# Optimization experiments

Hardware: AMD Instinct MI355X
Metric: run time of the kernel (lower is better)

## Reference

```python
import jax, jax.numpy as jnp
import numpy as np

D = 1024    # n_embd
H = 16      # n_heads
HD = D // H # head_dim
E = 8       # n_experts
K = 2       # k_best
DFF = 4096  # expert hidden
EPS = 1e-6
TEMP = 1.0  # target_temperature


def rmsnorm(x, w):
    return x * jax.lax.rsqrt(jnp.mean(x * x, axis=-1, keepdims=True) + EPS) * w


def setup_inputs() -> dict:
    key = jax.random.key(0)
    ks = jax.random.split(key, 10)
    B, S = 2, 2048
    s = 0.02
    return {
        "x": jax.random.normal(ks[0], (B, S, D), jnp.float32),
        "attention_mask": jnp.ones((B, S), jnp.int32),
        "attn_norm_w": jnp.ones((D,), jnp.float32),
        "wq": jax.random.normal(ks[1], (D, D), jnp.float32) * s,
        "wk": jax.random.normal(ks[2], (D, D), jnp.float32) * s,
        "wv": jax.random.normal(ks[3], (D, D), jnp.float32) * s,
        "wo": jax.random.normal(ks[4], (D, D), jnp.float32) * s,
        "mlp_norm_w": jnp.ones((D,), jnp.float32),
        "router_w": jax.random.normal(ks[5], (D, E), jnp.float32) * s,
        "w1": jax.random.normal(ks[6], (E, D, DFF), jnp.float32) * s,
        "b1": jnp.zeros((E, DFF), jnp.float32),
        "w2": jax.random.normal(ks[7], (E, DFF, D), jnp.float32) * s,
        "b2": jnp.zeros((E, D), jnp.float32),
    }


def reference(x, attention_mask, attn_norm_w, wq, wk, wv, wo, mlp_norm_w,
              router_w, w1, b1, w2, b2):
    B, S, _ = x.shape
    # ---- attention sub-block ----
    residual = x
    h = rmsnorm(x, attn_norm_w)
    q = (h @ wq).reshape(B, S, H, HD).transpose(0, 2, 1, 3)  # bhsd
    k = (h @ wk).reshape(B, S, H, HD).transpose(0, 2, 1, 3)
    v = (h @ wv).reshape(B, S, H, HD).transpose(0, 2, 1, 3)
    scores = jnp.einsum('bhqd,bhkd->bhqk', q, k) / np.sqrt(HD).astype(np.float32)
    causal = jnp.tril(jnp.ones((S, S), bool))
    mask = causal[None, None, :, :] & (attention_mask[:, None, None, :] > 0)
    scores = jnp.where(mask, scores, jnp.float32(-1e9))
    attn = jax.nn.softmax(scores, axis=-1)
    o = jnp.einsum('bhqk,bhkd->bhqd', attn, v).transpose(0, 2, 1, 3).reshape(B, S, D) @ wo
    x = residual + o

    # ---- MoE sub-block ----
    residual = x
    h = rmsnorm(x, mlp_norm_w)
    logits = h @ router_w                        # (B,S,E)
    probs = jax.nn.softmax(logits / TEMP, axis=-1)
    top_k_scores, top_k_indices = jax.lax.top_k(probs, K)  # (B,S,K)
    sel = jax.nn.one_hot(top_k_indices, E, dtype=probs.dtype)  # (B,S,K,E)
    expert_counts = sel.sum(axis=(0, 1, 2))      # (E,)
    frac = expert_counts / (B * S * K)
    balancing_loss = E * jnp.sum(frac * probs.mean(axis=(0, 1)))

    T = B * S
    flat = h.reshape(T, D)
    # dense per-expert MLP over all tokens, then gather the routed slots
    hid = jax.nn.gelu(jnp.einsum('td,edf->etf', flat, w1) + b1[:, None, :])  # (E,T,DFF)
    all_y = jnp.einsum('etf,efd->etd', hid, w2) + b2[:, None, :]             # (E,T,D)
    idx = top_k_indices.reshape(T, K)
    expert_out = all_y[idx, jnp.arange(T)[:, None], :]  # (T,K,D)
    # faithful to torch: outputs.view(k, B, S, D) is a raw reinterpretation
    out = expert_out.reshape(K, B, S, D)
    w = top_k_scores.transpose(2, 0, 1)[..., None]  # (K,B,S,1)
    x = residual + (out * w).sum(axis=0)
    return (x, balancing_loss, expert_counts)
```

## Files before the change

kernel.cpp:

```cpp
#include <hip/hip_runtime.h>


typedef _Float16 f16;
typedef _Float16 f16x8 __attribute__((ext_vector_type(8)));
typedef _Float16 f16x4v __attribute__((ext_vector_type(4)));
typedef float f32x4 __attribute__((ext_vector_type(4)));

#define DMODEL 1024
#define NHEAD  16
#define HDIM   64
#define NEXP   8
#define DFFN   4096
#define NBATCH 2
#define NSEQ   2048
#define NTOK   4096
#define NPAIR  8192

#define OFF_WQKVT  0ull
#define OFF_WOT    6291456ull
#define OFF_W1T    8388608ull
#define OFF_W2T    75497472ull
#define OFF_HATTN  142606336ull
#define OFF_Q      150994944ull
#define OFF_K      159383552ull
#define OFF_VT     167772160ull
#define OFF_OC     176160768ull
#define OFF_XMID   184549376ull
#define OFF_HMLP   201326592ull
#define OFF_HID    209715200ull
#define OFF_Y      276824064ull
#define OFF_Y2     OFF_HATTN
#define OFF_LIST   310378496ull
#define OFF_METAE  310509568ull
#define OFF_METAP  310542336ull
#define OFF_METAS  310575104ull
#define OFF_BPSUM  310607872ull
#define OFF_CNT    310640640ull
#define OFF_PSUM   310640704ull
#define OFF_BASE   310640768ull

__device__ __forceinline__ void ldsAsync16(const void* g, void* l) {
  __builtin_amdgcn_global_load_lds((const __attribute__((address_space(1))) void*)g,
                                   (__attribute__((address_space(3))) void*)l, 16, 0, 0);
}

__global__ void transpose_cast_kernel(const float* __restrict__ src, f16* __restrict__ dst,
                                      int R, int C) {
  __shared__ float tile[32][33];
  const size_t zoff = (size_t)blockIdx.z * R * C;
  src += zoff; dst += zoff;
  int c0 = blockIdx.x * 32, r0 = blockIdx.y * 32;
  int tx = threadIdx.x, ty = threadIdx.y;
#pragma unroll
  for (int i = 0; i < 4; i++)
    tile[ty + i * 8][tx] = src[(size_t)(r0 + ty + i * 8) * C + c0 + tx];
  __syncthreads();
#pragma unroll
  for (int i = 0; i < 4; i++)
    dst[(size_t)(c0 + ty + i * 8) * R + r0 + tx] = (f16)tile[tx][ty + i * 8];
}

__global__ void rmsnorm_kernel(const float* __restrict__ x, const float* __restrict__ w,
                               f16* __restrict__ out) {
  int t = blockIdx.x, tid = threadIdx.x;
  float4 v = ((const float4*)(x + (size_t)t * DMODEL))[tid];
  float ss = v.x * v.x + v.y * v.y + v.z * v.z + v.w * v.w;
#pragma unroll
  for (int o = 32; o > 0; o >>= 1) ss += __shfl_down(ss, o);
  __shared__ float red[4];
  if ((tid & 63) == 0) red[tid >> 6] = ss;
  __syncthreads();
  float tot = red[0] + red[1] + red[2] + red[3];
  float rstd = rsqrtf(tot / (float)DMODEL + 1e-6f);
  float4 wv = ((const float4*)w)[tid];
  f16x4v o4;
  o4[0] = (f16)(v.x * rstd * wv.x);
  o4[1] = (f16)(v.y * rstd * wv.y);
  o4[2] = (f16)(v.z * rstd * wv.z);
  o4[3] = (f16)(v.w * rstd * wv.w);
  *(f16x4v*)(out + (size_t)t * DMODEL + tid * 4) = o4;
}

template <class EPI>
__device__ __forceinline__ void gemm128(const f16* aP0, const f16* aP1, const f16* aP2, const f16* aP3,
                                        const f16* bP0, const f16* bP1, const f16* bP2, const f16* bP3,
                                        int K, EPI epi) {
  __shared__ __align__(16) f16 sA[128 * 64];
  __shared__ __align__(16) f16 sB[128 * 64];
  const int tid = threadIdx.x;
  const int lane = tid & 63, wave = tid >> 6;
  const int wm = (wave >> 1) * 64, wn = (wave & 1) * 64;
  const int q4 = lane >> 4, l15 = lane & 15;
  const int sw = lane & 7;
  const f16* aP[4] = {aP0, aP1, aP2, aP3};
  const f16* bP[4] = {bP0, bP1, bP2, bP3};
  f32x4 zero = {0.f, 0.f, 0.f, 0.f};
  f32x4 acc[4][4];
#pragma unroll
  for (int i = 0; i < 4; i++)
#pragma unroll
    for (int j = 0; j < 4; j++) acc[i][j] = zero;

  for (int k0 = 0; k0 < K; k0 += 64) {
    __syncthreads();
#pragma unroll
    for (int i = 0; i < 4; i++) {
      ldsAsync16(aP[i] + k0, &sA[(i * 4 + wave) * 512]);
      ldsAsync16(bP[i] + k0, &sB[(i * 4 + wave) * 512]);
    }
    __syncthreads();
#pragma unroll
    for (int kk = 0; kk < 2; kk++) {
      f16x8 af[4], bf[4];
      int jx = ((kk * 4 + q4) ^ sw) * 8;
#pragma unroll
      for (int mi = 0; mi < 4; mi++)
        af[mi] = *(const f16x8*)&sA[(wm + mi * 16 + l15) * 64 + jx];
#pragma unroll
      for (int ni = 0; ni < 4; ni++)
        bf[ni] = *(const f16x8*)&sB[(wn + ni * 16 + l15) * 64 + jx];
#pragma unroll
      for (int mi = 0; mi < 4; mi++)
#pragma unroll
        for (int ni = 0; ni < 4; ni++)
          acc[mi][ni] = __builtin_amdgcn_mfma_f32_16x16x32_f16(af[mi], bf[ni], acc[mi][ni], 0, 0, 0);
    }
  }
#pragma unroll
  for (int mi = 0; mi < 4; mi++)
#pragma unroll
    for (int ni = 0; ni < 4; ni++)
#pragma unroll
      for (int r = 0; r < 4; r++)
        epi(wm + mi * 16 + q4 * 4 + r, wn + ni * 16 + l15, acc[mi][ni][r]);
}

__global__ __launch_bounds__(256, 2) void gemm_qkv_kernel(
    const f16* __restrict__ hA, const f16* __restrict__ wT,
    f16* __restrict__ qb, f16* __restrict__ kb, f16* __restrict__ vtb) {
  int mt = blockIdx.y, nt = blockIdx.x;
  int tid = threadIdx.x, lane = tid & 63, wave = tid >> 6;
  int kc = lane & 7, rs = lane >> 3;
  int kcs = (kc ^ rs) * 8;
  const f16 *a[4], *b[4];
#pragma unroll
  for (int i = 0; i < 4; i++) {
    int row = i * 32 + wave * 8 + rs;
    a[i] = hA + (size_t)(mt * 128 + row) * DMODEL + kcs;
    b[i] = wT + (size_t)(nt * 128 + row) * DMODEL + kcs;
  }
  int mB = mt * 128, nB = nt * 128;
  gemm128(a[0], a[1], a[2], a[3], b[0], b[1], b[2], b[3], DMODEL,
    [&](int r, int c, float v) {
      int m = mB + r, n = nB + c;
      int mat = n >> 10, nn = n & 1023;
      int h = nn >> 6, d = nn & 63;
      int bI = m >> 11, s = m & 2047;
      int bh = bI * NHEAD + h;
      f16 hv = (f16)v;
      if (mat == 0)      qb[((size_t)bh * NSEQ + s) * HDIM + d] = hv;
      else if (mat == 1) kb[((size_t)bh * NSEQ + s) * HDIM + d] = hv;
      else               vtb[((size_t)bh * HDIM + d) * NSEQ + s] = hv;
    });
}

__global__ __launch_bounds__(256, 2) void gemm_o_kernel(
    const f16* __restrict__ oc, const f16* __restrict__ woT,
    const float* __restrict__ xin, float* __restrict__ xmid) {
  int mt = blockIdx.y, nt = blockIdx.x;
  int tid = threadIdx.x, lane = tid & 63, wave = tid >> 6;
  int kc = lane & 7, rs = lane >> 3;
  int kcs = (kc ^ rs) * 8;
  const f16 *a[4], *b[4];
#pragma unroll
  for (int i = 0; i < 4; i++) {
    int row = i * 32 + wave * 8 + rs;
    a[i] = oc + (size_t)(mt * 128 + row) * DMODEL + kcs;
    b[i] = woT + (size_t)(nt * 128 + row) * DMODEL + kcs;
  }
  int mB = mt * 128, nB = nt * 128;
  gemm128(a[0], a[1], a[2], a[3], b[0], b[1], b[2], b[3], DMODEL,
    [&](int r, int c, float v) {
      size_t idx = (size_t)(mB + r) * DMODEL + nB + c;
      xmid[idx] = xin[idx] + v;
    });
}

__global__ __launch_bounds__(256, 2) void gemm_moe1_kernel(
    const f16* __restrict__ hM, const f16* __restrict__ w1T, const float* __restrict__ b1,
    const int* __restrict__ cnt, const int* __restrict__ base, const int* __restrict__ list,
    f16* __restrict__ hid) {
  int e = blockIdx.z, mt = blockIdx.y, nt = blockIdx.x;
  int c_e = cnt[e];
  if (mt * 128 >= c_e) return;
  int tid = threadIdx.x, lane = tid & 63, wave = tid >> 6;
  int kc = lane & 7, rs = lane >> 3;
  int kcs = (kc ^ rs) * 8;
  const f16 *a[4], *b[4];
#pragma unroll
  for (int i = 0; i < 4; i++) {
    int row = i * 32 + wave * 8 + rs;
    int rr = mt * 128 + row; rr = rr < c_e ? rr : c_e - 1;
    int tok = list[e * NTOK + rr];
    a[i] = hM + (size_t)tok * DMODEL + kcs;
    b[i] = w1T + ((size_t)e * DFFN + nt * 128 + row) * DMODEL + kcs;
  }
  int rowBase = base[e] + mt * 128, nB = nt * 128, mLoc = mt * 128;
  gemm128(a[0], a[1], a[2], a[3], b[0], b[1], b[2], b[3], DMODEL,
    [&](int r, int c, float v) {
      if (mLoc + r < c_e) {
        float v2 = v + b1[e * DFFN + nB + c];
        float u = 1.5957691216057308f * (v2 + 0.044715f * v2 * v2 * v2);
        float th = 1.f - 2.f / (__expf(u) + 1.f);
        hid[(size_t)(rowBase + r) * DFFN + nB + c] = (f16)(0.5f * v2 * (1.f + th));
      }
    });
}

__global__ __launch_bounds__(256, 2) void gemm_moe2_kernel(
    const f16* __restrict__ hid, const f16* __restrict__ w2T, const float* __restrict__ b2,
    const int* __restrict__ cnt, const int* __restrict__ base,
    float* __restrict__ y, float* __restrict__ y2) {
  int z = blockIdx.z, e = z >> 1, kh = z & 1;
  int mt = blockIdx.y, nt = blockIdx.x;
  int c_e = cnt[e];
  if (mt * 128 >= c_e) return;
  int tid = threadIdx.x, lane = tid & 63, wave = tid >> 6;
  int kc = lane & 7, rs = lane >> 3;
  int kcs = (kc ^ rs) * 8 + kh * 2048;
  int bse = base[e];
  const f16 *a[4], *b[4];
#pragma unroll
  for (int i = 0; i < 4; i++) {
    int row = i * 32 + wave * 8 + rs;
    int rr = mt * 128 + row; rr = rr < c_e ? rr : c_e - 1;
    a[i] = hid + (size_t)(bse + rr) * DFFN + kcs;
    b[i] = w2T + ((size_t)e * DMODEL + nt * 128 + row) * DFFN + kcs;
  }
  int nB = nt * 128, mLoc = mt * 128;
  float* yo = kh ? y2 : y;
  gemm128(a[0], a[1], a[2], a[3], b[0], b[1], b[2], b[3], 2048,
    [&](int r, int c, float v) {
      if (mLoc + r < c_e) {
        float bias = kh ? 0.f : b2[e * DMODEL + nB + c];
        yo[(size_t)(bse + mLoc + r) * DMODEL + nB + c] = v + bias;
      }
    });
}

__global__ __launch_bounds__(256, 4) void attn_kernel(
    const f16* __restrict__ qb, const f16* __restrict__ kb, const f16* __restrict__ vtb,
    const int* __restrict__ amask, f16* __restrict__ oc) {
  int bh = blockIdx.x, qt = blockIdx.y;
  int bI = bh >> 4, h = bh & 15;
  int qbase = qt * 64;
  int tid = threadIdx.x, lane = tid & 63, wave = tid >> 6;
  int q4 = lane >> 4, l15 = lane & 15;
  int kc = lane & 7, rs = lane >> 3;

  __shared__ __align__(16) f16 sQ[64 * 64];
  __shared__ __align__(16) f16 sK[64 * 64];
  __shared__ __align__(16) f16 sVT[64 * 64];
  __shared__ __align__(16) f16 sP[4][16 * 64];
  __shared__ int sMask[64];

  const f16* qBH = qb + (size_t)bh * NSEQ * HDIM;
  const f16* kBH = kb + (size_t)bh * NSEQ * HDIM;
  const f16* vBH = vtb + (size_t)bh * HDIM * NSEQ;

#pragma unroll
  for (int i = 0; i < 2; i++) {
    int row = i * 32 + wave * 8 + rs;
    ldsAsync16(qBH + (size_t)(qbase + row) * HDIM + kc * 8, &sQ[(i * 4 + wave) * 512]);
  }

  f32x4 zero = {0.f, 0.f, 0.f, 0.f};
  f32x4 accO[4];
  float mrow[4], lrow[4];
#pragma unroll
  for (int j = 0; j < 4; j++) { accO[j] = zero; mrow[j] = -3.0e38f; lrow[j] = 0.f; }

  f16* sPw = sP[wave];

  for (int kt = 0; kt <= qt; kt++) {
    int kb0 = kt * 64;
    bool diag = (kt == qt);
    __syncthreads();
#pragma unroll
    for (int i = 0; i < 2; i++) {
      int row = i * 32 + wave * 8 + rs;
      ldsAsync16(kBH + (size_t)(kb0 + row) * HDIM + kc * 8, &sK[(i * 4 + wave) * 512]);
      ldsAsync16(vBH + (size_t)row * NSEQ + kb0 + kc * 8, &sVT[(i * 4 + wave) * 512]);
    }
    if (tid < 64) sMask[tid] = amask[bI * NSEQ + kb0 + tid];
    __syncthreads();

    f32x4 accS[4];
#pragma unroll
    for (int j = 0; j < 4; j++) accS[j] = zero;
#pragma unroll
    for (int kk = 0; kk < 2; kk++) {
      f16x8 af = *(const f16x8*)&sQ[(wave * 16 + l15) * 64 + kk * 32 + q4 * 8];
      f16x8 bf[4];
#pragma unroll
      for (int nj = 0; nj < 4; nj++)
        bf[nj] = *(const f16x8*)&sK[(nj * 16 + l15) * 64 + kk * 32 + q4 * 8];
#pragma unroll
      for (int nj = 0; nj < 4; nj++)
        accS[nj] = __builtin_amdgcn_mfma_f32_16x16x32_f16(af, bf[nj], accS[nj], 0, 0, 0);
    }
    bool mok[4];
    int gk[4];
#pragma unroll
    for (int nj = 0; nj < 4; nj++) {
      gk[nj] = nj * 16 + l15;
      mok[nj] = sMask[gk[nj]] > 0;
    }
#pragma unroll
    for (int r = 0; r < 4; r++) {
      int lq = wave * 16 + q4 * 4 + r;
      float rm = -3.0e38f;
#pragma unroll
      for (int nj = 0; nj < 4; nj++) {
        float s = accS[nj][r] * 0.125f;
        bool ok = mok[nj] && (!diag || gk[nj] <= lq);
        s = ok ? s : -1.0e9f;
        accS[nj][r] = s;
        rm = fmaxf(rm, s);
      }
#pragma unroll
      for (int o = 1; o < 16; o <<= 1) rm = fmaxf(rm, __shfl_xor(rm, o));
      float mold = mrow[r];
      float mnew = fmaxf(mold, rm);
      float alpha = __expf(mold - mnew);
      float rsum = 0.f;
#pragma unroll
      for (int nj = 0; nj < 4; nj++) {
        float p = __expf(accS[nj][r] - mnew);
        rsum += p;
        sPw[(q4 * 4 + r) * 64 + nj * 16 + l15] = (f16)p;
      }
#pragma unroll
      for (int o = 1; o < 16; o <<= 1) rsum += __shfl_xor(rsum, o);
      lrow[r] = lrow[r] * alpha + rsum;
      mrow[r] = mnew;
#pragma unroll
      for (int dj = 0; dj < 4; dj++) accO[dj][r] *= alpha;
    }
#pragma unroll
    for (int kk = 0; kk < 2; kk++) {
      f16x8 pf = *(const f16x8*)&sPw[l15 * 64 + kk * 32 + q4 * 8];
      f16x8 vf[4];
#pragma unroll
      for (int dj = 0; dj < 4; dj++)
        vf[dj] = *(const f16x8*)&sVT[(dj * 16 + l15) * 64 + kk * 32 + q4 * 8];
#pragma unroll
      for (int dj = 0; dj < 4; dj++)
        accO[dj] = __builtin_amdgcn_mfma_f32_16x16x32_f16(pf, vf[dj], accO[dj], 0, 0, 0);
    }
  }
#pragma unroll
  for (int r = 0; r < 4; r++) {
    float inv = 1.f / lrow[r];
    int s = qbase + wave * 16 + q4 * 4 + r;
    size_t rowoff = ((size_t)bI * NSEQ + s) * DMODEL + h * HDIM;
#pragma unroll
    for (int dj = 0; dj < 4; dj++)
      oc[rowoff + dj * 16 + l15] = (f16)(accO[dj][r] * inv);
  }
}

__global__ __launch_bounds__(256) void router_kernel(
    const float* __restrict__ xmid, const float* __restrict__ normw,
    const float* __restrict__ rw, int2* __restrict__ metaE,
    float2* __restrict__ metaS, float* __restrict__ blockpsum) {
  int wave = threadIdx.x >> 6, lane = threadIdx.x & 63;
  int t = blockIdx.x * 4 + wave;
  __shared__ float sprob[4][8];

  const float4* xr = (const float4*)(xmid + (size_t)t * DMODEL);
  const float4* wr = (const float4*)normw;
  float4 v[4];
  float ss = 0.f;
#pragma unroll
  for (int i = 0; i < 4; i++) {
    v[i] = xr[lane * 4 + i];
    ss += v[i].x * v[i].x + v[i].y * v[i].y + v[i].z * v[i].z + v[i].w * v[i].w;
  }
#pragma unroll
  for (int o = 32; o > 0; o >>= 1) ss += __shfl_xor(ss, o);
  float rstd = rsqrtf(ss / (float)DMODEL + 1e-6f);

  float part[8] = {0, 0, 0, 0, 0, 0, 0, 0};
#pragma unroll
  for (int i = 0; i < 4; i++) {
    float4 wv = wr[lane * 4 + i];
    float hv[4] = {v[i].x * rstd * wv.x, v[i].y * rstd * wv.y,
                   v[i].z * rstd * wv.z, v[i].w * rstd * wv.w};
#pragma unroll
    for (int j = 0; j < 4; j++) {
      int row = lane * 16 + i * 4 + j;
      const float4* rr = (const float4*)(rw + (size_t)row * NEXP);
      float4 a = rr[0], b = rr[1];
      part[0] += hv[j] * a.x; part[1] += hv[j] * a.y;
      part[2] += hv[j] * a.z; part[3] += hv[j] * a.w;
      part[4] += hv[j] * b.x; part[5] += hv[j] * b.y;
      part[6] += hv[j] * b.z; part[7] += hv[j] * b.w;
    }
  }
#pragma unroll
  for (int o = 1; o < 64; o <<= 1)
#pragma unroll
    for (int e = 0; e < 8; e++) part[e] += __shfl_xor(part[e], o);

  if (lane == 0) {
    float mx = -3.0e38f;
#pragma unroll
    for (int e = 0; e < 8; e++) mx = fmaxf(mx, part[e]);
    float probs[8], sum = 0.f;
#pragma unroll
    for (int e = 0; e < 8; e++) { probs[e] = __expf(part[e] - mx); sum += probs[e]; }
    float inv = 1.f / sum;
#pragma unroll
    for (int e = 0; e < 8; e++) { probs[e] *= inv; sprob[wave][e] = probs[e]; }
    int e0 = 0;
#pragma unroll
    for (int e = 1; e < 8; e++) if (part[e] > part[e0]) e0 = e;
    int e1 = (e0 == 0) ? 1 : 0;
#pragma unroll
    for (int e = 0; e < 8; e++) if (e != e0 && part[e] > part[e1]) e1 = e;
    metaE[t] = make_int2(e0, e1);
    metaS[t] = make_float2(probs[e0], probs[e1]);
  }
  __syncthreads();
  if (threadIdx.x < 8)
    blockpsum[blockIdx.x * 8 + threadIdx.x] =
        sprob[0][threadIdx.x] + sprob[1][threadIdx.x] +
        sprob[2][threadIdx.x] + sprob[3][threadIdx.x];
}

__global__ __launch_bounds__(256) void scatter_kernel(
    const int2* __restrict__ metaE, int* __restrict__ list,
    int* __restrict__ metaP, int* __restrict__ cnt) {
  int e = blockIdx.x;
  int tid = threadIdx.x, lane = tid & 63, w = tid >> 6;
  __shared__ int wsum[4];
  __shared__ int sbase;
  if (tid == 0) sbase = 0;
  __syncthreads();
  for (int c = 0; c < NTOK; c += 256) {
    int tok = c + tid;
    int2 me = metaE[tok];
    bool m0 = (me.x == e), m1 = (me.y == e);
    bool m = m0 || m1;
    unsigned long long mask = __ballot(m);
    int wpre = __popcll(mask & ((1ull << lane) - 1ull));
    if (lane == 0) wsum[w] = __popcll(mask);
    __syncthreads();
    int base0 = sbase;
    int pre = wpre;
    for (int i = 0; i < w; i++) pre += wsum[i];
    int tot = wsum[0] + wsum[1] + wsum[2] + wsum[3];
    if (m) {
      int pos = base0 + pre;
      list[e * NTOK + base0 + pre] = tok;
      metaP[tok * 2 + (m0 ? 0 : 1)] = pos;
    }
    __syncthreads();
    if (tid == 0) sbase = base0 + tot;
  }
  __syncthreads();
  if (tid == 0) cnt[e] = sbase;
}

__global__ __launch_bounds__(256) void finalize_kernel(
    const int* __restrict__ cnt, const float* __restrict__ blockpsum,
    int* __restrict__ base, float* __restrict__ out_tail) {
  int tid = threadIdx.x;
  int e = tid & 7, slot = tid >> 3;
  float acc = 0.f;
  for (int i = slot; i < 1024; i += 32) acc += blockpsum[i * 8 + e];
  __shared__ float red[256];
  red[tid] = acc;
  __syncthreads();
  for (int s = 128; s >= 8; s >>= 1) {
    if (tid < s) red[tid] += red[tid + s];
    __syncthreads();
  }
  if (tid == 0) {
    int b = 0;
#pragma unroll
    for (int i = 0; i < 8; i++) { base[i] = b; b += cnt[i]; }
    base[8] = b;
    float loss = 0.f;
#pragma unroll
    for (int i = 0; i < 8; i++)
      loss += ((float)cnt[i] / (float)NPAIR) * (red[i] / (float)NTOK);
    out_tail[0] = loss * (float)NEXP;
#pragma unroll
    for (int i = 0; i < 8; i++) out_tail[1 + i] = (float)cnt[i];
  }
}

__global__ void combine_kernel(const float* __restrict__ xmid, const float* __restrict__ yv,
                               const float* __restrict__ yv2,
                               const int2* __restrict__ metaE, const int* __restrict__ metaP,
                               const float2* __restrict__ metaS,
                               const int* __restrict__ base, float* __restrict__ out) {
  int t = blockIdx.x, tid = threadIdx.x;
  int2 me = metaE[t];
  float2 sc = metaS[t];
  size_t s0 = (size_t)(base[me.x] + metaP[t * 2 + 0]) * DMODEL;
  size_t s1 = (size_t)(base[me.y] + metaP[t * 2 + 1]) * DMODEL;
  float4 a = ((const float4*)(xmid + (size_t)t * DMODEL))[tid];
  float4 y0a = ((const float4*)(yv + s0))[tid];
  float4 y0b = ((const float4*)(yv2 + s0))[tid];
  float4 y1a = ((const float4*)(yv + s1))[tid];
  float4 y1b = ((const float4*)(yv2 + s1))[tid];
  float4 o;
  o.x = a.x + sc.x * (y0a.x + y0b.x) + sc.y * (y1a.x + y1b.x);
  o.y = a.y + sc.x * (y0a.y + y0b.y) + sc.y * (y1a.y + y1b.y);
  o.z = a.z + sc.x * (y0a.z + y0b.z) + sc.y * (y1a.z + y1b.z);
  o.w = a.w + sc.x * (y0a.w + y0b.w) + sc.y * (y1a.w + y1b.w);
  ((float4*)(out + (size_t)t * DMODEL))[tid] = o;
}

extern "C" void kernel_launch(void* const* d_in, const int* in_sizes, int n_in,
                              void* d_out, int out_size, void* d_ws, size_t ws_size,
                              hipStream_t stream) {
  (void)in_sizes; (void)n_in; (void)out_size; (void)ws_size;
  const float* x    = (const float*)d_in[0];
  const int*   am   = (const int*)d_in[1];
  const float* anw  = (const float*)d_in[2];
  const float* wq   = (const float*)d_in[3];
  const float* wk   = (const float*)d_in[4];
  const float* wv   = (const float*)d_in[5];
  const float* wo   = (const float*)d_in[6];
  const float* mnw  = (const float*)d_in[7];
  const float* rw   = (const float*)d_in[8];
  const float* w1   = (const float*)d_in[9];
  const float* b1   = (const float*)d_in[10];
  const float* w2   = (const float*)d_in[11];
  const float* b2   = (const float*)d_in[12];
  float* out = (float*)d_out;
  char* ws = (char*)d_ws;

  f16* wqkvT = (f16*)(ws + OFF_WQKVT);
  f16* woT   = (f16*)(ws + OFF_WOT);
  f16* w1T   = (f16*)(ws + OFF_W1T);
  f16* w2T   = (f16*)(ws + OFF_W2T);
  f16* hattn = (f16*)(ws + OFF_HATTN);
  f16* qb    = (f16*)(ws + OFF_Q);
  f16* kb    = (f16*)(ws + OFF_K);
  f16* vtb   = (f16*)(ws + OFF_VT);
  f16* oc    = (f16*)(ws + OFF_OC);
  float* xmid = (float*)(ws + OFF_XMID);
  f16* hmlp  = (f16*)(ws + OFF_HMLP);
  f16* hid   = (f16*)(ws + OFF_HID);
  float* y   = (float*)(ws + OFF_Y);
  float* y2  = (float*)(ws + OFF_Y2);
  int* list  = (int*)(ws + OFF_LIST);
  int2* metaE = (int2*)(ws + OFF_METAE);
  int* metaP  = (int*)(ws + OFF_METAP);
  float2* metaS = (float2*)(ws + OFF_METAS);
  float* bpsum = (float*)(ws + OFF_BPSUM);
  int* cnt   = (int*)(ws + OFF_CNT);
  int* base  = (int*)(ws + OFF_BASE);

  dim3 tb(32, 8, 1);
  transpose_cast_kernel<<<dim3(32, 32, 1), tb, 0, stream>>>(wq, wqkvT, 1024, 1024);
  transpose_cast_kernel<<<dim3(32, 32, 1), tb, 0, stream>>>(wk, wqkvT + 1024 * 1024, 1024, 1024);
  transpose_cast_kernel<<<dim3(32, 32, 1), tb, 0, stream>>>(wv, wqkvT + 2 * 1024 * 1024, 1024, 1024);
  transpose_cast_kernel<<<dim3(32, 32, 1), tb, 0, stream>>>(wo, woT, 1024, 1024);
  transpose_cast_kernel<<<dim3(128, 32, 8), tb, 0, stream>>>(w1, w1T, 1024, 4096);
  transpose_cast_kernel<<<dim3(32, 128, 8), tb, 0, stream>>>(w2, w2T, 4096, 1024);

  rmsnorm_kernel<<<NTOK, 256, 0, stream>>>(x, anw, hattn);
  gemm_qkv_kernel<<<dim3(24, 32), 256, 0, stream>>>(hattn, wqkvT, qb, kb, vtb);
  attn_kernel<<<dim3(32, 32), 256, 0, stream>>>(qb, kb, vtb, am, oc);
  gemm_o_kernel<<<dim3(8, 32), 256, 0, stream>>>(oc, woT, x, xmid);
  rmsnorm_kernel<<<NTOK, 256, 0, stream>>>(xmid, mnw, hmlp);
  router_kernel<<<1024, 256, 0, stream>>>(xmid, mnw, rw, metaE, metaS, bpsum);
  scatter_kernel<<<8, 256, 0, stream>>>(metaE, list, metaP, cnt);
  finalize_kernel<<<1, 256, 0, stream>>>(cnt, bpsum, base, out + (size_t)NTOK * DMODEL);
  gemm_moe1_kernel<<<dim3(32, 32, 8), 256, 0, stream>>>(hmlp, w1T, b1, cnt, base, list, hid);
  gemm_moe2_kernel<<<dim3(8, 32, 16), 256, 0, stream>>>(hid, w2T, b2, cnt, base, y, y2);
  combine_kernel<<<NTOK, 256, 0, stream>>>(xmid, y, y2, metaE, metaP, metaS, base, out);
}
```

Measured before the change: 851.2 us.

## Use 256x256 tiles with 8 waves for the first MoE expert GEMM

```diff
diff --git a/kernel.cpp b/kernel.cpp
--- a/kernel.cpp
+++ b/kernel.cpp
@@ -135,6 +135,68 @@
         epi(wm + mi * 16 + q4 * 4 + r, wn + ni * 16 + l15, acc[mi][ni][r]);
 }
 
+template <class EPI>
+__device__ __forceinline__ void gemm256(const f16* const aP[4], const f16* const bP[4],
+                                        int K, EPI epi) {
+  __shared__ __align__(16) f16 sA[2][256 * 64];
+  __shared__ __align__(16) f16 sB[2][256 * 64];
+  const int tid = threadIdx.x;
+  const int lane = tid & 63, wave = tid >> 6;
+  const int wm = (wave >> 2) * 128, wn = (wave & 3) * 64;
+  const int q4 = lane >> 4, l15 = lane & 15;
+  const int sw = l15 & 7;
+  const int ldsBase = wave * 512;
+  f32x4 zero = {0.f, 0.f, 0.f, 0.f};
+  f32x4 acc[8][4];
+#pragma unroll
+  for (int i = 0; i < 8; i++)
+#pragma unroll
+    for (int j = 0; j < 4; j++) acc[i][j] = zero;
+
+#pragma unroll
+  for (int i = 0; i < 4; i++) {
+    ldsAsync16(aP[i], &sA[0][i * 4096 + ldsBase]);
+    ldsAsync16(bP[i], &sB[0][i * 4096 + ldsBase]);
+  }
+  __syncthreads();
+
+  int cur = 0;
+  for (int k0 = 64; k0 <= K; k0 += 64) {
+    if (k0 < K) {
+#pragma unroll
+      for (int i = 0; i < 4; i++) {
+        ldsAsync16(aP[i] + k0, &sA[cur ^ 1][i * 4096 + ldsBase]);
+        ldsAsync16(bP[i] + k0, &sB[cur ^ 1][i * 4096 + ldsBase]);
+      }
+    }
+#pragma unroll
+    for (int kk = 0; kk < 2; kk++) {
+      f16x8 af[8], bf[4];
+      int jx = ((kk * 4 + q4) ^ sw) * 8;
+#pragma unroll
+      for (int ni = 0; ni < 4; ni++)
+        bf[ni] = *(const f16x8*)&sB[cur][(wn + ni * 16 + l15) * 64 + jx];
+#pragma unroll
+      for (int mi = 0; mi < 8; mi++)
+        af[mi] = *(const f16x8*)&sA[cur][(wm + mi * 16 + l15) * 64 + jx];
+#pragma unroll
+      for (int mi = 0; mi < 8; mi++)
+#pragma unroll
+        for (int ni = 0; ni < 4; ni++)
+          acc[mi][ni] = __builtin_amdgcn_mfma_f32_16x16x32_f16(af[mi], bf[ni], acc[mi][ni], 0, 0, 0);
+    }
+    __syncthreads();
+    cur ^= 1;
+  }
+#pragma unroll
+  for (int mi = 0; mi < 8; mi++)
+#pragma unroll
+    for (int ni = 0; ni < 4; ni++)
+#pragma unroll
+      for (int r = 0; r < 4; r++)
+        epi(wm + mi * 16 + q4 * 4 + r, wn + ni * 16 + l15, acc[mi][ni][r]);
+}
+
 __global__ __launch_bounds__(256, 2) void gemm_qkv_kernel(
     const f16* __restrict__ hA, const f16* __restrict__ wT,
     f16* __restrict__ qb, f16* __restrict__ kb, f16* __restrict__ vtb) {
@@ -186,27 +248,28 @@
     });
 }
 
-__global__ __launch_bounds__(256, 2) void gemm_moe1_kernel(
+__global__ __launch_bounds__(512, 2) void gemm_moe1_kernel(
     const f16* __restrict__ hM, const f16* __restrict__ w1T, const float* __restrict__ b1,
     const int* __restrict__ cnt, const int* __restrict__ base, const int* __restrict__ list,
     f16* __restrict__ hid) {
   int e = blockIdx.z, mt = blockIdx.y, nt = blockIdx.x;
   int c_e = cnt[e];
-  if (mt * 128 >= c_e) return;
+  if (mt * 256 >= c_e) return;
   int tid = threadIdx.x, lane = tid & 63, wave = tid >> 6;
-  int kc = lane & 7, rs = lane >> 3;
-  int kcs = (kc ^ rs) * 8;
-  const f16 *a[4], *b[4];
+  int kc = lane & 7, rs8 = lane >> 3;
+  int kcs = (kc ^ rs8) * 8;
+  const f16* a[4];
+  const f16* b[4];
 #pragma unroll
   for (int i = 0; i < 4; i++) {
-    int row = i * 32 + wave * 8 + rs;
-    int rr = mt * 128 + row; rr = rr < c_e ? rr : c_e - 1;
+    int row = i * 64 + wave * 8 + rs8;
+    int rr = mt * 256 + row; rr = rr < c_e ? rr : c_e - 1;
     int tok = list[e * NTOK + rr];
     a[i] = hM + (size_t)tok * DMODEL + kcs;
-    b[i] = w1T + ((size_t)e * DFFN + nt * 128 + row) * DMODEL + kcs;
-  }
-  int rowBase = base[e] + mt * 128, nB = nt * 128, mLoc = mt * 128;
-  gemm128(a[0], a[1], a[2], a[3], b[0], b[1], b[2], b[3], DMODEL,
+    b[i] = w1T + ((size_t)e * DFFN + nt * 256 + row) * DMODEL + kcs;
+  }
+  int rowBase = base[e] + mt * 256, nB = nt * 256, mLoc = mt * 256;
+  gemm256(a, b, DMODEL,
     [&](int r, int c, float v) {
       if (mLoc + r < c_e) {
         float v2 = v + b1[e * DFFN + nB + c];
@@ -583,7 +646,7 @@
   router_kernel<<<1024, 256, 0, stream>>>(xmid, mnw, rw, metaE, metaS, bpsum);
   scatter_kernel<<<8, 256, 0, stream>>>(metaE, list, metaP, cnt);
   finalize_kernel<<<1, 256, 0, stream>>>(cnt, bpsum, base, out + (size_t)NTOK * DMODEL);
-  gemm_moe1_kernel<<<dim3(32, 32, 8), 256, 0, stream>>>(hmlp, w1T, b1, cnt, base, list, hid);
+  gemm_moe1_kernel<<<dim3(16, 16, 8), 512, 0, stream>>>(hmlp, w1T, b1, cnt, base, list, hid);
   gemm_moe2_kernel<<<dim3(8, 32, 16), 256, 0, stream>>>(hid, w2T, b2, cnt, base, y, y2);
   combine_kernel<<<NTOK, 256, 0, stream>>>(xmid, y, y2, metaE, metaP, metaS, base, out);
 }
```

After: 882.5 us. 1.04x slower.
